# Performance work log

Hardware: AMD Instinct MI355X
Metric: run time of the kernel (lower is better)

The kernel has to match this reference:

```python
import jax, jax.numpy as jnp
import numpy as np
from jax import lax

B, A, SEQ, FIN = 512, 16, 50, 6
H, H2, T, G, S = 256, 128, 60, 64, 6
GR0, GR1 = -50.0, 50.0
CELL = (GR1 - GR0) / G
NTYPES, EMB = 10, 16
NENC, NL = 5, 2

def setup_inputs() -> dict:
    key = jax.random.key(0)
    ks = jax.random.split(key, 40)
    def rn(k, shape, scale=0.05):
        return (jax.random.normal(k, shape) * scale).astype(jnp.float32)
    history = jax.random.normal(ks[0], (B, A, SEQ, FIN), dtype=jnp.float32)
    types = jax.random.randint(ks[1], (B,), 0, NTYPES)
    history = history.at[:, 0, 0, 5].set(types.astype(jnp.float32))
    d = dict(history=history)
    d['emb'] = rn(ks[2], (NTYPES, EMB))
    d['fe_W1'] = rn(ks[3], (FIN + EMB, H)); d['fe_b1'] = jnp.zeros((H,), jnp.float32)
    d['fe_W2'] = rn(ks[4], (H, H));        d['fe_b2'] = jnp.zeros((H,), jnp.float32)
    d['enc_Wih'] = rn(ks[5], (NENC, NL, H, 3 * H))
    d['enc_Whh'] = rn(ks[6], (NENC, NL, H, 3 * H))
    d['enc_bih'] = rn(ks[7], (NENC, NL, 3 * H))
    d['enc_bhh'] = rn(ks[8], (NENC, NL, 3 * H))
    d['dec_Wih0'] = rn(ks[9], (2, 3 * H)); d['dec_Whh0'] = rn(ks[10], (H, 3 * H))
    d['dec_bih0'] = rn(ks[11], (3 * H));   d['dec_bhh0'] = rn(ks[12], (3 * H))
    d['dec_Wih1'] = rn(ks[13], (H, 3 * H)); d['dec_Whh1'] = rn(ks[14], (H, 3 * H))
    d['dec_bih1'] = rn(ks[15], (3 * H));    d['dec_bhh1'] = rn(ks[16], (3 * H))
    d['hg_W1'] = rn(ks[17], (H, H));   d['hg_b1'] = jnp.zeros((H,), jnp.float32)
    d['hg_W2'] = rn(ks[18], (H, H2));  d['hg_b2'] = jnp.zeros((H2,), jnp.float32)
    d['hg_W3'] = rn(ks[19], (H2, T * 2)); d['hg_b3'] = jnp.zeros((T * 2,), jnp.float32)
    d['ce_W1'] = rn(ks[20], (H, H2));  d['ce_b1'] = jnp.zeros((H2,), jnp.float32)
    d['ce_W2'] = rn(ks[21], (H2, T));  d['ce_b2'] = jnp.zeros((T,), jnp.float32)
    d['hp_W1'] = rn(ks[22], (H, H));   d['hp_b1'] = jnp.zeros((H,), jnp.float32)
    d['hp_W2'] = rn(ks[23], (H, G * G)); d['hp_b2'] = jnp.zeros((G * G,), jnp.float32)
    return d

def _gru_cell(xt, h, Wih, Whh, bih, bhh):
    # torch GRU gate order: r, z, n
    gi = xt @ Wih + bih
    gh = h @ Whh + bhh
    Hd = h.shape[-1]
    r = jax.nn.sigmoid(gi[:, :Hd] + gh[:, :Hd])
    z = jax.nn.sigmoid(gi[:, Hd:2 * Hd] + gh[:, Hd:2 * Hd])
    n = jnp.tanh(gi[:, 2 * Hd:] + r * gh[:, 2 * Hd:])
    return (1.0 - z) * n + z * h

def _forward(history, emb, fe_W1, fe_b1, fe_W2, fe_b2,
             enc_Wih, enc_Whh, enc_bih, enc_bhh,
             dec_Wih0, dec_Whh0, dec_bih0, dec_bhh0,
             dec_Wih1, dec_Whh1, dec_bih1, dec_bhh1,
             hg_W1, hg_b1, hg_W2, hg_b2, hg_W3, hg_b3,
             ce_W1, ce_b1, ce_W2, ce_b2, hp_W1, hp_b1, hp_W2, hp_b2):
    ego = history[:, 0]                                   # [B,SEQ,6]
    etype = jnp.clip(ego[:, 0, 5].astype(jnp.int32), 0, 9)
    # type -> encoder index (vehicle,pedestrian,cyclist,bus,default)
    eidx = jnp.array([0, 1, 4, 2, 3, 4, 4, 4, 4, 4], jnp.int32)[etype]
    te = emb[etype]                                       # [B,16]
    x_in = jnp.concatenate([ego, jnp.broadcast_to(te[:, None, :], (B, SEQ, EMB))], axis=-1)
    feat = jax.nn.relu(x_in @ fe_W1 + fe_b1) @ fe_W2 + fe_b2  # [B,SEQ,H]

    # 2-layer GRU with per-example (type-gathered) weights
    x_cur = feat.transpose(1, 0, 2)                       # [SEQ,B,H]
    h_finals = []
    for l in range(NL):
        Wih = enc_Wih[eidx, l]; Whh = enc_Whh[eidx, l]    # [B,H,3H]
        bih = enc_bih[eidx, l]; bhh = enc_bhh[eidx, l]    # [B,3H]
        def step(h, xt, Wih=Wih, Whh=Whh, bih=bih, bhh=bhh):
            gi = jnp.einsum('bd,bdg->bg', xt, Wih) + bih
            gh = jnp.einsum('bh,bhg->bg', h, Whh) + bhh
            r = jax.nn.sigmoid(gi[:, :H] + gh[:, :H])
            z = jax.nn.sigmoid(gi[:, H:2 * H] + gh[:, H:2 * H])
            n = jnp.tanh(gi[:, 2 * H:] + r * gh[:, 2 * H:])
            hn = (1.0 - z) * n + z * h
            return hn, hn
        h_last, ys = lax.scan(step, jnp.zeros((B, H), feat.dtype), x_cur)
        x_cur = ys
        h_finals.append(h_last)
    enc_h0, enc_h1 = h_finals

    # decoder GRU, single timestep: x = last ego position
    x0 = ego[:, -1, :2]
    h0 = _gru_cell(x0, enc_h0, dec_Wih0, dec_Whh0, dec_bih0, dec_bhh0)
    h1 = _gru_cell(h0, enc_h1, dec_Wih1, dec_Whh1, dec_bih1, dec_bhh1)
    last_hidden = h1                                      # [B,H]

    traj = (jax.nn.relu(jax.nn.relu(last_hidden @ hg_W1 + hg_b1) @ hg_W2 + hg_b2) @ hg_W3 + hg_b3)
    traj = traj.reshape(B, T, 2)
    conf = jax.nn.relu(last_hidden @ ce_W1 + ce_b1) @ ce_W2 + ce_b2   # [B,T]

    key = jax.random.key(42)
    k_noise, k_samp = jax.random.split(key)
    noise = jax.random.normal(k_noise, (T, B, H), last_hidden.dtype)
    scale = (0.1 * jnp.arange(T, dtype=last_hidden.dtype) / T)[:, None, None]
    th = last_hidden[None] + noise * scale                # [T,B,H]
    logits = jax.nn.relu(th @ hp_W1 + hp_b1) @ hp_W2 + hp_b2  # [T,B,G*G]

    # vectorized multinomial over (samples, timesteps, batch)
    idx = jax.random.categorical(k_samp, logits, shape=(S - 1, T, B))  # int [S-1,T,B]
    x_idx = (idx % G).astype(jnp.float32)
    y_idx = (idx // G).astype(jnp.float32)
    pts = jnp.stack([GR0 + x_idx * CELL + CELL / 2,
                     GR0 + y_idx * CELL + CELL / 2], axis=-1)  # [S-1,T,B,2]
    pts = pts.transpose(2, 0, 1, 3)                       # [B,S-1,T,2]

    predictions = jnp.concatenate([traj[:, None], pts], axis=1)  # [B,S,T,2]
    decay = jnp.float32(0.9) ** jnp.arange(S, dtype=jnp.float32)
    confidences = conf.mean(axis=1)[:, None] * decay[None, :]    # [B,S]
    return predictions, confidences

def reference(history, emb, fe_W1, fe_b1, fe_W2, fe_b2,
              enc_Wih, enc_Whh, enc_bih, enc_bhh,
              dec_Wih0, dec_Whh0, dec_bih0, dec_bhh0,
              dec_Wih1, dec_Whh1, dec_bih1, dec_bhh1,
              hg_W1, hg_b1, hg_W2, hg_b2, hg_W3, hg_b3,
              ce_W1, ce_b1, ce_W2, ce_b2, hp_W1, hp_b1, hp_W2, hp_b2):
    return _forward(history, emb, fe_W1, fe_b1, fe_W2, fe_b2,
                    enc_Wih, enc_Whh, enc_bih, enc_bhh,
                    dec_Wih0, dec_Whh0, dec_bih0, dec_bhh0,
                    dec_Wih1, dec_Whh1, dec_bih1, dec_bhh1,
                    hg_W1, hg_b1, hg_W2, hg_b2, hg_W3, hg_b3,
                    ce_W1, ce_b1, ce_W2, ce_b2, hp_W1, hp_b1, hp_W2, hp_b2)
```

## Files before the change

### kernel.cpp

```cpp
#include <hip/hip_runtime.h>
#include <stdint.h>
#include <math.h>

#define JAX_PARTITIONABLE 1

#define B_ 512
#define SEQ_ 50
#define H_ 256
#define H2_ 128
#define T_ 60
#define S_ 6
#define EMB_ 16
#define NL_ 2
#define TG_ 768
#define CAT_ 4096
#define GUMBEL_N 629145600u
#define NOISE_N 7864320u

__host__ __device__ inline void tf2x32(uint32_t k0, uint32_t k1, uint32_t x0, uint32_t x1,
                                       uint32_t& o0, uint32_t& o1) {
  uint32_t ks2 = k0 ^ k1 ^ 0x1BD11BDAu;
  x0 += k0; x1 += k1;
#define TFR(r) do { x0 += x1; x1 = (x1 << r) | (x1 >> (32 - r)); x1 ^= x0; } while (0)
  TFR(13); TFR(15); TFR(26); TFR(6);
  x0 += k1; x1 += ks2 + 1u;
  TFR(17); TFR(29); TFR(16); TFR(24);
  x0 += ks2; x1 += k0 + 2u;
  TFR(13); TFR(15); TFR(26); TFR(6);
  x0 += k0; x1 += k1 + 3u;
  TFR(17); TFR(29); TFR(16); TFR(24);
  x0 += k1; x1 += ks2 + 4u;
  TFR(13); TFR(15); TFR(26); TFR(6);
  x0 += ks2; x1 += k0 + 5u;
#undef TFR
  o0 = x0; o1 = x1;
}

__device__ inline uint32_t jax_bits(uint32_t k0, uint32_t k1, uint32_t i, uint32_t n) {
#if JAX_PARTITIONABLE
  (void)n;
  uint32_t a, b;
  tf2x32(k0, k1, 0u, i, a, b);
  return a ^ b;
#else
  uint32_t half = n >> 1;
  uint32_t lo = (i < half) ? i : (i - half);
  uint32_t a, b;
  tf2x32(k0, k1, lo, lo + half, a, b);
  return (i < half) ? a : b;
#endif
}

__device__ inline float bits_to_f01(uint32_t bits) {
  return __uint_as_float((bits >> 9) | 0x3f800000u) - 1.0f;
}

__device__ inline float erfinv_f(float x) {
  double xd = (double)x;
  float w = (float)(-log((1.0 - xd) * (1.0 + xd)));
  float p;
  if (w < 5.0f) {
    w = __fadd_rn(w, -2.5f);
    p = 2.81022636e-08f;
    p = __fadd_rn(3.43273939e-07f, __fmul_rn(p, w));
    p = __fadd_rn(-3.5233877e-06f, __fmul_rn(p, w));
    p = __fadd_rn(-4.39150654e-06f, __fmul_rn(p, w));
    p = __fadd_rn(0.00021858087f, __fmul_rn(p, w));
    p = __fadd_rn(-0.00125372503f, __fmul_rn(p, w));
    p = __fadd_rn(-0.00417768164f, __fmul_rn(p, w));
    p = __fadd_rn(0.246640727f, __fmul_rn(p, w));
    p = __fadd_rn(1.50140941f, __fmul_rn(p, w));
  } else {
    w = __fadd_rn(__fsqrt_rn(w), -3.0f);
    p = -0.000200214257f;
    p = __fadd_rn(0.000100950558f, __fmul_rn(p, w));
    p = __fadd_rn(0.00134934322f, __fmul_rn(p, w));
    p = __fadd_rn(-0.00367342844f, __fmul_rn(p, w));
    p = __fadd_rn(0.00573950773f, __fmul_rn(p, w));
    p = __fadd_rn(-0.0076224613f, __fmul_rn(p, w));
    p = __fadd_rn(0.00943887047f, __fmul_rn(p, w));
    p = __fadd_rn(1.00167406f, __fmul_rn(p, w));
    p = __fadd_rn(2.83297682f, __fmul_rn(p, w));
  }
  return __fmul_rn(p, x);
}

__device__ inline float gumbel_f32(uint32_t bits) {
  float f = bits_to_f01(bits);
  float u = fmaxf(f, 1.17549435e-38f);
  float l1 = logf(u);
  float g = -logf(-l1);
  return g;
}

__device__ inline uint32_t orderkey(float s) {
  uint32_t sb = __float_as_uint(s);
  return (sb & 0x80000000u) ? ~sb : (sb | 0x80000000u);
}

__global__ __launch_bounds__(512) void k_init(const float* __restrict__ hist,
                                              float* __restrict__ x0buf, int* __restrict__ ip) {
  int b = threadIdx.x;
  if (b < B_) {
    float tv = hist[b * 4800 + 5];
    int et = (int)tv;
    et = et < 0 ? 0 : (et > 9 ? 9 : et);
    const int mp[10] = {0, 1, 4, 2, 3, 4, 4, 4, 4, 4};
    ip[b] = et;
    ip[512 + b] = mp[et];
    x0buf[b * 2 + 0] = hist[b * 4800 + 49 * 6 + 0];
    x0buf[b * 2 + 1] = hist[b * 4800 + 49 * 6 + 1];
  }
  __syncthreads();
  if (b == 0) {
    int cnt[5] = {0, 0, 0, 0, 0};
    for (int i = 0; i < B_; i++) cnt[ip[512 + i]]++;
    int off[6];
    off[0] = 0;
    for (int e = 0; e < 5; e++) off[e + 1] = off[e] + cnt[e];
    int pos[5];
    for (int e = 0; e < 5; e++) pos[e] = off[e];
    for (int i = 0; i < B_; i++) { int e = ip[512 + i]; ip[1024 + pos[e]++] = i; }
    int* tbl = ip + 1536;
    int nrt = 0;
    for (int e = 0; e < 5; e++) {
      int n = cnt[e];
      for (int s = 0; s < n; s += 16) {
        tbl[1 + nrt] = e;
        tbl[37 + nrt] = off[e] + s;
        tbl[73 + nrt] = (n - s) < 16 ? (n - s) : 16;
        nrt++;
      }
    }
    tbl[0] = nrt;
  }
}

__global__ void k_zero(uint32_t* p, int n) {
  int i = blockIdx.x * blockDim.x + threadIdx.x;
  if (i < n) p[i] = 0u;
}

__global__ __launch_bounds__(256) void k_feat(const float* __restrict__ hist, const float* __restrict__ emb,
    const float* __restrict__ W1, const float* __restrict__ b1,
    const float* __restrict__ W2, const float* __restrict__ b2,
    const int* __restrict__ ip, float* __restrict__ featbuf) {
  __shared__ float xs[16][22];
  __shared__ float t1[16][H_];
  int row0 = blockIdx.x * 16;
  int tid = threadIdx.x;
  for (int idx = tid; idx < 16 * 22; idx += 256) {
    int r = idx / 22, c = idx % 22;
    int g = row0 + r;
    int b = g / SEQ_, s = g % SEQ_;
    xs[r][c] = (c < 6) ? hist[b * 4800 + s * 6 + c] : emb[ip[b] * EMB_ + (c - 6)];
  }
  __syncthreads();
  int j = tid;
  {
    double acc[16];
    for (int r = 0; r < 16; r++) acc[r] = 0.0;
    for (int k = 0; k < 22; k++) {
      double w = (double)W1[k * H_ + j];
      for (int r = 0; r < 16; r++) acc[r] += (double)xs[r][k] * w;
    }
    double bb = (double)b1[j];
    for (int r = 0; r < 16; r++) t1[r][j] = fmaxf((float)(acc[r] + bb), 0.0f);
  }
  __syncthreads();
  {
    double acc[16];
    for (int r = 0; r < 16; r++) acc[r] = 0.0;
    for (int k = 0; k < H_; k++) {
      double w = (double)W2[k * H_ + j];
      for (int r = 0; r < 16; r++) acc[r] += (double)t1[r][k] * w;
    }
    double bb = (double)b2[j];
    for (int r = 0; r < 16; r++) {
      float v = (float)(acc[r] + bb);
      int g = row0 + r;
      int b = g / SEQ_, s = g % SEQ_;
      featbuf[(size_t)s * (B_ * H_) + (size_t)b * H_ + j] = v;
    }
  }
}

__device__ __forceinline__ void gi_block(float (*xs)[H_], int* rowb,
    int rt, int cg, int tid,
    const float* __restrict__ x, float* __restrict__ gi_out,
    const float* __restrict__ Wih_base, const float* __restrict__ bih_base,
    int layer, const int* __restrict__ ip) {
  const int* tbl = ip + 1536;
  const int* order = ip + 1024;
  int nrt = tbl[0];
  if (rt >= nrt) return;
  int e = tbl[1 + rt];
  int start = tbl[37 + rt];
  int nr = tbl[73 + rt];
  for (int idx = tid; idx < 16 * H_; idx += 256) {
    int r = idx >> 8, k = idx & 255;
    int rr = (r < nr) ? r : 0;
    int b = order[start + rr];
    if (k == 0) rowb[r] = b;
    xs[r][k] = x[b * H_ + k];
  }
  __syncthreads();
  size_t woff = (size_t)(e * NL_ + layer);
  const float* Wih = Wih_base + woff * (size_t)H_ * TG_;
  const float* bih = bih_base + woff * TG_;
  int j = tid & 31, rs = tid >> 5;
  int c = cg * 32 + j;
  int cr = c, cz = H_ + c, cn = 2 * H_ + c;
  double ar0 = 0, ar1 = 0, az0 = 0, az1 = 0, an0 = 0, an1 = 0;
  for (int k = 0; k < H_; k++) {
    float wr = Wih[k * TG_ + cr], wz = Wih[k * TG_ + cz], wn = Wih[k * TG_ + cn];
    float x0 = xs[rs][k], x1 = xs[rs + 8][k];
    ar0 += (double)x0 * wr; ar1 += (double)x1 * wr;
    az0 += (double)x0 * wz; az1 += (double)x1 * wz;
    an0 += (double)x0 * wn; an1 += (double)x1 * wn;
  }
  double br = (double)bih[cr], bz = (double)bih[cz], bn = (double)bih[cn];
  for (int p = 0; p < 2; p++) {
    int r = rs + 8 * p;
    if (r >= nr) continue;
    int b = rowb[r];
    gi_out[b * TG_ + cr] = (float)((p ? ar1 : ar0) + br);
    gi_out[b * TG_ + cz] = (float)((p ? az1 : az0) + bz);
    gi_out[b * TG_ + cn] = (float)((p ? an1 : an0) + bn);
  }
}

__device__ __forceinline__ void step_block(float (*hs)[H_], int* rowb,
    int rt, int cg, int tid,
    const float* __restrict__ gi_in, const float* __restrict__ hin,
    float* __restrict__ hout, float* __restrict__ ys,
    const float* __restrict__ Whh_base, const float* __restrict__ bhh_base,
    int layer, const int* __restrict__ ip) {
  const int* tbl = ip + 1536;
  const int* order = ip + 1024;
  int nrt = tbl[0];
  if (rt >= nrt) return;
  int e = tbl[1 + rt];
  int start = tbl[37 + rt];
  int nr = tbl[73 + rt];
  for (int idx = tid; idx < 16 * H_; idx += 256) {
    int r = idx >> 8, k = idx & 255;
    int rr = (r < nr) ? r : 0;
    int b = order[start + rr];
    if (k == 0) rowb[r] = b;
    hs[r][k] = hin[b * H_ + k];
  }
  __syncthreads();
  size_t woff = (size_t)(e * NL_ + layer);
  const float* Whh = Whh_base + woff * (size_t)H_ * TG_;
  const float* bhh = bhh_base + woff * TG_;
  int j = tid & 31, rs = tid >> 5;
  int c = cg * 32 + j;
  int cr = c, cz = H_ + c, cn = 2 * H_ + c;
  double gr0 = 0, gr1 = 0, gz0 = 0, gz1 = 0, gn0 = 0, gn1 = 0;
  for (int k = 0; k < H_; k++) {
    float wr = Whh[k * TG_ + cr], wz = Whh[k * TG_ + cz], wn = Whh[k * TG_ + cn];
    float h0 = hs[rs][k], h1 = hs[rs + 8][k];
    gr0 += (double)h0 * wr; gr1 += (double)h1 * wr;
    gz0 += (double)h0 * wz; gz1 += (double)h1 * wz;
    gn0 += (double)h0 * wn; gn1 += (double)h1 * wn;
  }
  double bhr = (double)bhh[cr], bhz = (double)bhh[cz], bhn = (double)bhh[cn];
  for (int p = 0; p < 2; p++) {
    int r = rs + 8 * p;
    if (r >= nr) continue;
    int b = rowb[r];
    double gir = (double)gi_in[b * TG_ + cr];
    double giz = (double)gi_in[b * TG_ + cz];
    double gin = (double)gi_in[b * TG_ + cn];
    double ghr = (p ? gr1 : gr0) + bhr;
    double ghz = (p ? gz1 : gz0) + bhz;
    double ghn = (p ? gn1 : gn0) + bhn;
    double rr = 1.0 / (1.0 + exp(-(gir + ghr)));
    double zz = 1.0 / (1.0 + exp(-(giz + ghz)));
    double nn = tanh(gin + rr * ghn);
    double hv = (double)hs[r][c];
    float hnew = (float)((1.0 - zz) * nn + zz * hv);
    hout[b * H_ + c] = hnew;
    if (ys) ys[b * H_ + c] = hnew;
  }
}

__global__ __launch_bounds__(256) void k_pipe(int d,
    const float* __restrict__ feat, float* __restrict__ ys0,
    float* __restrict__ gi0, float* __restrict__ gi1,
    float* __restrict__ h0A, float* __restrict__ h0B,
    float* __restrict__ h1A, float* __restrict__ h1B,
    const float* __restrict__ Wih, const float* __restrict__ Whh,
    const float* __restrict__ bih, const float* __restrict__ bhh,
    const int* __restrict__ ip) {
  __shared__ float sb[16][H_];
  __shared__ int rowb[16];
  int g = blockIdx.x;
  int grp = g / 288, bx = g % 288;
  int rt = bx >> 3, cg = bx & 7;
  int tid = threadIdx.x;
  if (grp == 0) {
    int t = d; if (t >= SEQ_) return;
    gi_block(sb, rowb, rt, cg, tid, feat + (size_t)t * 131072,
             gi0 + (size_t)(t & 1) * 393216, Wih, bih, 0, ip);
  } else if (grp == 1) {
    int t = d - 1; if (t < 0 || t >= SEQ_) return;
    const float* hin = (t & 1) ? h0B : h0A;
    float* hout = (t & 1) ? h0A : h0B;
    step_block(sb, rowb, rt, cg, tid, gi0 + (size_t)(t & 1) * 393216,
               hin, hout, ys0 + (size_t)t * 131072, Whh, bhh, 0, ip);
  } else if (grp == 2) {
    int t = d - 2; if (t < 0 || t >= SEQ_) return;
    gi_block(sb, rowb, rt, cg, tid, ys0 + (size_t)t * 131072,
             gi1 + (size_t)(t & 1) * 393216, Wih, bih, 1, ip);
  } else {
    int t = d - 3; if (t < 0 || t >= SEQ_) return;
    const float* hin = (t & 1) ? h1B : h1A;
    float* hout = (t & 1) ? h1A : h1B;
    step_block(sb, rowb, rt, cg, tid, gi1 + (size_t)(t & 1) * 393216,
               hin, hout, nullptr, Whh, bhh, 1, ip);
  }
}

template <int D1>
__global__ __launch_bounds__(256) void k_gru(
    const float* __restrict__ x, const float* __restrict__ hin,
    float* __restrict__ hout,
    const float* __restrict__ Wih, const float* __restrict__ Whh,
    const float* __restrict__ bih, const float* __restrict__ bhh) {
  __shared__ float xs[16][(D1 == 2) ? 2 : H_];
  __shared__ float hs[16][H_];
  int bx = blockIdx.x, by = blockIdx.y;
  int start = bx * 16;
  int tid = threadIdx.x;
  for (int idx = tid; idx < 16 * H_; idx += 256) {
    int r = idx >> 8, k = idx & 255;
    int b = start + r;
    hs[r][k] = hin[b * H_ + k];
    if (D1 == H_) xs[r][k] = x[b * H_ + k];
    else if (k < D1) xs[r][k] = x[b * D1 + k];
  }
  __syncthreads();
  int j = tid & 31, rs = tid >> 5;
  int hc = by * 32 + j;
  int cr = hc, cz = H_ + hc, cn = 2 * H_ + hc;
  double ra0 = 0, ra1 = 0, za0 = 0, za1 = 0, ni0 = 0, ni1 = 0, nh0 = 0, nh1 = 0;
  for (int k = 0; k < H_; k++) {
    float wrh = Whh[k * TG_ + cr], wzh = Whh[k * TG_ + cz], wnh = Whh[k * TG_ + cn];
    float h0v = hs[rs][k], h1v = hs[rs + 8][k];
    ra0 += (double)h0v * wrh; ra1 += (double)h1v * wrh;
    za0 += (double)h0v * wzh; za1 += (double)h1v * wzh;
    nh0 += (double)h0v * wnh; nh1 += (double)h1v * wnh;
    if (D1 == H_) {
      float wri = Wih[k * TG_ + cr], wzi = Wih[k * TG_ + cz], wni = Wih[k * TG_ + cn];
      float x0v = xs[rs][k], x1v = xs[rs + 8][k];
      ra0 += (double)x0v * wri; ra1 += (double)x1v * wri;
      za0 += (double)x0v * wzi; za1 += (double)x1v * wzi;
      ni0 += (double)x0v * wni; ni1 += (double)x1v * wni;
    }
  }
  if (D1 != H_) {
    for (int k = 0; k < D1; k++) {
      float wri = Wih[k * TG_ + cr], wzi = Wih[k * TG_ + cz], wni = Wih[k * TG_ + cn];
      float x0v = xs[rs][k], x1v = xs[rs + 8][k];
      ra0 += (double)x0v * wri; ra1 += (double)x1v * wri;
      za0 += (double)x0v * wzi; za1 += (double)x1v * wzi;
      ni0 += (double)x0v * wni; ni1 += (double)x1v * wni;
    }
  }
  double br_i = (double)bih[cr], bz_i = (double)bih[cz], bn_i = (double)bih[cn];
  double br_h = (double)bhh[cr], bz_h = (double)bhh[cz], bn_h = (double)bhh[cn];
  for (int p = 0; p < 2; p++) {
    int r = rs + 8 * p;
    double ra = p ? ra1 : ra0, za = p ? za1 : za0, ni = p ? ni1 : ni0, nh = p ? nh1 : nh0;
    double rr = 1.0 / (1.0 + exp(-(ra + br_i + br_h)));
    double zz = 1.0 / (1.0 + exp(-(za + bz_i + bz_h)));
    double nn = tanh((ni + bn_i) + rr * (nh + bn_h));
    double hv = (double)hs[r][hc];
    float hnew = (float)((1.0 - zz) * nn + zz * hv);
    hout[(start + r) * H_ + hc] = hnew;
  }
}

__global__ __launch_bounds__(256) void k_heads(const float* __restrict__ lh,
    const float* __restrict__ hgW1, const float* __restrict__ hgb1,
    const float* __restrict__ hgW2, const float* __restrict__ hgb2,
    const float* __restrict__ hgW3, const float* __restrict__ hgb3,
    const float* __restrict__ ceW1, const float* __restrict__ ceb1,
    const float* __restrict__ ceW2, const float* __restrict__ ceb2,
    float* __restrict__ out) {
  __shared__ float hsm[16][H_];
  __shared__ float t1[16][H_];
  __shared__ float t2[16][H2_];
  __shared__ float c2s[16][T_];
  int row0 = blockIdx.x * 16;
  int tid = threadIdx.x;
  for (int idx = tid; idx < 16 * H_; idx += 256) {
    int r = idx >> 8, k = idx & 255;
    hsm[r][k] = lh[(size_t)(row0 + r) * H_ + k];
  }
  __syncthreads();
  {
    int j = tid;
    for (int r = 0; r < 16; r++) {
      double a = 0;
      for (int k = 0; k < H_; k++) a += (double)hsm[r][k] * (double)hgW1[k * H_ + j];
      t1[r][j] = fmaxf((float)(a + (double)hgb1[j]), 0.0f);
    }
  }
  __syncthreads();
  if (tid < H2_) {
    int j = tid;
    for (int r = 0; r < 16; r++) {
      double a = 0;
      for (int k = 0; k < H_; k++) a += (double)t1[r][k] * (double)hgW2[k * H2_ + j];
      t2[r][j] = fmaxf((float)(a + (double)hgb2[j]), 0.0f);
    }
  }
  __syncthreads();
  if (tid < 2 * T_) {
    int j = tid;
    for (int r = 0; r < 16; r++) {
      double a = 0;
      for (int k = 0; k < H2_; k++) a += (double)t2[r][k] * (double)hgW3[k * (2 * T_) + j];
      float v = (float)(a + (double)hgb3[j]);
      int b = row0 + r;
      int t = j >> 1, c = j & 1;
      out[(((size_t)b * S_ + 0) * T_ + t) * 2 + c] = v;
    }
  }
  __syncthreads();
  if (tid < H2_) {
    int j = tid;
    for (int r = 0; r < 16; r++) {
      double a = 0;
      for (int k = 0; k < H_; k++) a += (double)hsm[r][k] * (double)ceW1[k * H2_ + j];
      t2[r][j] = fmaxf((float)(a + (double)ceb1[j]), 0.0f);
    }
  }
  __syncthreads();
  if (tid < T_) {
    int j = tid;
    for (int r = 0; r < 16; r++) {
      double a = 0;
      for (int k = 0; k < H2_; k++) a += (double)t2[r][k] * (double)ceW2[k * T_ + j];
      c2s[r][j] = (float)(a + (double)ceb2[j]);
    }
  }
  __syncthreads();
  if (tid < 16) {
    int r = tid;
    int b = row0 + r;
    double s = 0;
    for (int j = 0; j < T_; j++) s += (double)c2s[r][j];
    float m = (float)(s / 60.0);
    for (int sd = 0; sd < S_; sd++) {
      float d = (float)pow((double)0.9f, (double)sd);
      out[368640 + b * S_ + sd] = __fmul_rn(m, d);
    }
  }
}

__global__ __launch_bounds__(256) void k_hp1(const float* __restrict__ lh,
    const float* __restrict__ W1, const float* __restrict__ b1,
    float* __restrict__ h1buf, uint32_t nk0, uint32_t nk1) {
  __shared__ float th[16][H_];
  int row0 = blockIdx.x * 16;
  int tid = threadIdx.x;
  const float SQRT2F = 1.4142135623730951f;
  const float LO = -0x1.fffffep-1f;
  for (int idx = tid; idx < 16 * H_; idx += 256) {
    int r = idx >> 8, k = idx & 255;
    int g = row0 + r;
    int t = g / B_, b = g % B_;
    uint32_t i = ((uint32_t)t * B_ + (uint32_t)b) * H_ + (uint32_t)k;
    uint32_t bits = jax_bits(nk0, nk1, i, NOISE_N);
    float f = bits_to_f01(bits);
    float u = fmaxf(LO, __fadd_rn(__fmul_rn(f, 2.0f), LO));
    float nz = __fmul_rn(SQRT2F, erfinv_f(u));
    float sc = __fdiv_rn(__fmul_rn(0.1f, (float)t), 60.0f);
    th[r][k] = __fadd_rn(lh[(size_t)b * H_ + k], __fmul_rn(nz, sc));
  }
  __syncthreads();
  int j = tid;
  double acc[16];
  for (int r = 0; r < 16; r++) acc[r] = 0.0;
  for (int k = 0; k < H_; k++) {
    double w = (double)W1[k * H_ + j];
    for (int r = 0; r < 16; r++) acc[r] += (double)th[r][k] * w;
  }
  double bb = (double)b1[j];
  for (int r = 0; r < 16; r++)
    h1buf[(size_t)(row0 + r) * H_ + j] = fmaxf((float)(acc[r] + bb), 0.0f);
}

__global__ __launch_bounds__(256) void k_hp2(const float* __restrict__ h1buf,
    const float* __restrict__ W2, const float* __restrict__ b2,
    unsigned long long* __restrict__ samples, uint32_t sk0, uint32_t sk1) {
  __shared__ float h1[16][H_];
  int row0 = blockIdx.x * 16;
  int cat0 = blockIdx.y * 128;
  int tid = threadIdx.x;
  for (int idx = tid; idx < 16 * H_ / 4; idx += 256) {
    int r = idx >> 6, k4 = (idx & 63) << 2;
    *(float4*)&h1[r][k4] = *(const float4*)&h1buf[(size_t)(row0 + r) * H_ + k4];
  }
  __syncthreads();
  int wave = tid >> 6;
  int lane = tid & 63;
  int catA = cat0 + 2 * lane;
  int rbase = 4 * wave;

  float acc[4][2];
  for (int q = 0; q < 4; q++) { acc[q][0] = 0.0f; acc[q][1] = 0.0f; }
  const float* w2p = W2 + catA;
  for (int k = 0; k < H_; k += 4) {
    float4 hv0 = *(const float4*)&h1[rbase + 0][k];
    float4 hv1 = *(const float4*)&h1[rbase + 1][k];
    float4 hv2 = *(const float4*)&h1[rbase + 2][k];
    float4 hv3 = *(const float4*)&h1[rbase + 3][k];
#pragma unroll
    for (int kk = 0; kk < 4; kk++) {
      float2 w = *(const float2*)&w2p[(size_t)(k + kk) * CAT_];
      float h0 = (&hv0.x)[kk], h1v = (&hv1.x)[kk], h2 = (&hv2.x)[kk], h3 = (&hv3.x)[kk];
      acc[0][0] = __fmaf_rn(h0, w.x, acc[0][0]); acc[0][1] = __fmaf_rn(h0, w.y, acc[0][1]);
      acc[1][0] = __fmaf_rn(h1v, w.x, acc[1][0]); acc[1][1] = __fmaf_rn(h1v, w.y, acc[1][1]);
      acc[2][0] = __fmaf_rn(h2, w.x, acc[2][0]); acc[2][1] = __fmaf_rn(h2, w.y, acc[2][1]);
      acc[3][0] = __fmaf_rn(h3, w.x, acc[3][0]); acc[3][1] = __fmaf_rn(h3, w.y, acc[3][1]);
    }
  }
  float lg[4][2];
  float b0 = b2[catA], b1v = b2[catA + 1];
  for (int q = 0; q < 4; q++) {
    lg[q][0] = __fadd_rn(acc[q][0], b0);
    lg[q][1] = __fadd_rn(acc[q][1], b1v);
  }

  int t = row0 / B_;
  int bbase = row0 % B_;
#pragma unroll
  for (int s = 0; s < S_ - 1; s++) {
#pragma unroll
    for (int q = 0; q < 4; q++) {
      int brow = bbase + rbase + q;
      uint32_t ibase = (((uint32_t)s * T_ + (uint32_t)t) * B_ + (uint32_t)brow) * CAT_ + (uint32_t)catA;
      float g0 = gumbel_f32(jax_bits(sk0, sk1, ibase, GUMBEL_N));
      float g1 = gumbel_f32(jax_bits(sk0, sk1, ibase + 1u, GUMBEL_N));
      float s0 = __fadd_rn(g0, lg[q][0]);
      float s1 = __fadd_rn(g1, lg[q][1]);
      uint32_t k0 = orderkey(s0), k1 = orderkey(s1);
      uint32_t bestk; int bestc;
      if (k1 > k0) { bestk = k1; bestc = catA + 1; }
      else         { bestk = k0; bestc = catA; }
      uint32_t m = bestk;
      for (int off = 1; off < 64; off <<= 1) {
        uint32_t o = __shfl_xor(m, off, 64);
        m = m > o ? m : o;
      }
      unsigned long long mask = __ballot(bestk == m);
      int src = __ffsll(mask) - 1;
      int wcat = __shfl(bestc, src, 64);
      if (lane == 0) {
        unsigned long long p =
            (((unsigned long long)m) << 32) | (unsigned long long)(~(uint32_t)wcat);
        atomicMax(&samples[((size_t)s * T_ + t) * B_ + brow], p);
      }
    }
  }
}

__global__ void k_emit(const unsigned long long* __restrict__ samples, float* __restrict__ out) {
  int gid = blockIdx.x * blockDim.x + threadIdx.x;
  if (gid >= (S_ - 1) * T_ * B_) return;
  int b = gid % B_;
  int t = (gid / B_) % T_;
  int s = gid / (B_ * T_);
  unsigned long long v = samples[gid];
  uint32_t cat = ~(uint32_t)(v & 0xFFFFFFFFu);
  float xi = (float)(cat & 63u);
  float yi = (float)(cat >> 6);
  float px = -50.0f + xi * 1.5625f + 0.78125f;
  float py = -50.0f + yi * 1.5625f + 0.78125f;
  size_t o = (((size_t)b * S_ + (size_t)(s + 1)) * T_ + t) * 2;
  out[o] = px;
  out[o + 1] = py;
}

extern "C" void kernel_launch(void* const* d_in, const int* in_sizes, int n_in,
                              void* d_out, int out_size, void* d_ws, size_t ws_size,
                              hipStream_t stream) {
  (void)in_sizes; (void)n_in; (void)out_size; (void)ws_size;
  const float* hist   = (const float*)d_in[0];
  const float* emb    = (const float*)d_in[1];
  const float* feW1   = (const float*)d_in[2];
  const float* feb1   = (const float*)d_in[3];
  const float* feW2   = (const float*)d_in[4];
  const float* feb2   = (const float*)d_in[5];
  const float* encWih = (const float*)d_in[6];
  const float* encWhh = (const float*)d_in[7];
  const float* encbih = (const float*)d_in[8];
  const float* encbhh = (const float*)d_in[9];
  const float* dWih0  = (const float*)d_in[10];
  const float* dWhh0  = (const float*)d_in[11];
  const float* dbih0  = (const float*)d_in[12];
  const float* dbhh0  = (const float*)d_in[13];
  const float* dWih1  = (const float*)d_in[14];
  const float* dWhh1  = (const float*)d_in[15];
  const float* dbih1  = (const float*)d_in[16];
  const float* dbhh1  = (const float*)d_in[17];
  const float* hgW1   = (const float*)d_in[18];
  const float* hgb1   = (const float*)d_in[19];
  const float* hgW2   = (const float*)d_in[20];
  const float* hgb2   = (const float*)d_in[21];
  const float* hgW3   = (const float*)d_in[22];
  const float* hgb3   = (const float*)d_in[23];
  const float* ceW1   = (const float*)d_in[24];
  const float* ceb1   = (const float*)d_in[25];
  const float* ceW2   = (const float*)d_in[26];
  const float* ceb2   = (const float*)d_in[27];
  const float* hpW1   = (const float*)d_in[28];
  const float* hpb1   = (const float*)d_in[29];
  const float* hpW2   = (const float*)d_in[30];
  const float* hpb2   = (const float*)d_in[31];
  float* out = (float*)d_out;
  float* ws = (float*)d_ws;

  float* feat  = ws;
  float* ys0   = ws + 6553600;
  float* gi0   = ws + 13107200;
  float* gi1   = ws + 13893632;
  float* h0A   = ws + 14680064;
  float* h0B   = h0A + 131072;
  float* h1A   = h0B + 131072;
  float* h1B   = h1A + 131072;
  float* dech0 = h1B + 131072;
  float* lh    = dech0 + 131072;
  float* x0buf = lh + 131072;
  int*   ip    = (int*)(x0buf + 1024);
  unsigned long long* samples =
      (unsigned long long*)(((uintptr_t)(ip + 2048) + 255) & ~(uintptr_t)255);
  float* h1hp  = ws;

  uint32_t kn0, kn1, ks0, ks1;
#if JAX_PARTITIONABLE
  tf2x32(0u, 42u, 0u, 0u, kn0, kn1);
  tf2x32(0u, 42u, 0u, 1u, ks0, ks1);
#else
  { uint32_t a0, a1, b0, b1;
    tf2x32(0u, 42u, 0u, 2u, a0, a1);
    tf2x32(0u, 42u, 1u, 3u, b0, b1);
    kn0 = a0; kn1 = b0; ks0 = a1; ks1 = b1; }
#endif

  k_init<<<dim3(1), dim3(512), 0, stream>>>(hist, x0buf, ip);
  k_zero<<<dim3((524288 + 255) / 256), dim3(256), 0, stream>>>((uint32_t*)h0A, 524288);
  k_zero<<<dim3((307200 + 255) / 256), dim3(256), 0, stream>>>((uint32_t*)samples, 307200);
  k_feat<<<dim3(1600), dim3(256), 0, stream>>>(hist, emb, feW1, feb1, feW2, feb2, ip, feat);

  for (int d = 0; d < SEQ_ + 3; d++) {
    k_pipe<<<dim3(1152), dim3(256), 0, stream>>>(d,
        feat, ys0, gi0, gi1, h0A, h0B, h1A, h1B,
        encWih, encWhh, encbih, encbhh, ip);
  }

  k_gru<2><<<dim3(32, 8), dim3(256), 0, stream>>>(
      x0buf, h0A, dech0, dWih0, dWhh0, dbih0, dbhh0);
  k_gru<H_><<<dim3(32, 8), dim3(256), 0, stream>>>(
      dech0, h1A, lh, dWih1, dWhh1, dbih1, dbhh1);

  k_heads<<<dim3(32), dim3(256), 0, stream>>>(lh, hgW1, hgb1, hgW2, hgb2, hgW3, hgb3,
                                              ceW1, ceb1, ceW2, ceb2, out);
  k_hp1<<<dim3(1920), dim3(256), 0, stream>>>(lh, hpW1, hpb1, h1hp, kn0, kn1);
  k_hp2<<<dim3(1920, 32), dim3(256), 0, stream>>>(h1hp, hpW2, hpb2, samples, ks0, ks1);
  k_emit<<<dim3(600), dim3(256), 0, stream>>>(samples, out);
}
```

Baseline: 6.115 ms.

## Widen hp2 tiles to four categories per lane with packed FMA and alignbit rotates

```diff
diff --git a/kernel.cpp b/kernel.cpp
--- a/kernel.cpp
+++ b/kernel.cpp
@@ -17,11 +17,26 @@
 #define GUMBEL_N 629145600u
 #define NOISE_N 7864320u
 
+typedef float f32x2 __attribute__((ext_vector_type(2)));
+
+#define PKFMA_LO(acc, w, h) \
+  asm("v_pk_fma_f32 %0, %1, %2, %0 op_sel:[0,0,0] op_sel_hi:[1,0,1]" : "+v"(acc) : "v"(w), "v"(h))
+#define PKFMA_HI(acc, w, h) \
+  asm("v_pk_fma_f32 %0, %1, %2, %0 op_sel:[0,1,0] op_sel_hi:[1,1,1]" : "+v"(acc) : "v"(w), "v"(h))
+
+__host__ __device__ inline uint32_t rotl32(uint32_t x, int r) {
+#if defined(__HIP_DEVICE_COMPILE__)
+  return __builtin_amdgcn_alignbit(x, x, 32 - r);
+#else
+  return (x << r) | (x >> (32 - r));
+#endif
+}
+
 __host__ __device__ inline void tf2x32(uint32_t k0, uint32_t k1, uint32_t x0, uint32_t x1,
                                        uint32_t& o0, uint32_t& o1) {
   uint32_t ks2 = k0 ^ k1 ^ 0x1BD11BDAu;
   x0 += k0; x1 += k1;
-#define TFR(r) do { x0 += x1; x1 = (x1 << r) | (x1 >> (32 - r)); x1 ^= x0; } while (0)
+#define TFR(r) do { x0 += x1; x1 = rotl32(x1, r); x1 ^= x0; } while (0)
   TFR(13); TFR(15); TFR(26); TFR(6);
   x0 += k1; x1 += ks2 + 1u;
   TFR(17); TFR(29); TFR(16); TFR(24);
@@ -89,8 +104,7 @@
   float f = bits_to_f01(bits);
   float u = fmaxf(f, 1.17549435e-38f);
   float l1 = logf(u);
-  float g = -logf(-l1);
-  return g;
+  return -logf(-l1);
 }
 
 __device__ inline uint32_t orderkey(float s) {
@@ -500,7 +514,7 @@
     unsigned long long* __restrict__ samples, uint32_t sk0, uint32_t sk1) {
   __shared__ float h1[16][H_];
   int row0 = blockIdx.x * 16;
-  int cat0 = blockIdx.y * 128;
+  int cat0 = blockIdx.y * 256;
   int tid = threadIdx.x;
   for (int idx = tid; idx < 16 * H_ / 4; idx += 256) {
     int r = idx >> 6, k4 = (idx & 63) << 2;
@@ -509,32 +523,44 @@
   __syncthreads();
   int wave = tid >> 6;
   int lane = tid & 63;
-  int catA = cat0 + 2 * lane;
+  int catA = cat0 + 4 * lane;
   int rbase = 4 * wave;
 
-  float acc[4][2];
-  for (int q = 0; q < 4; q++) { acc[q][0] = 0.0f; acc[q][1] = 0.0f; }
+  f32x2 acc[4][2];
+#pragma unroll
+  for (int r = 0; r < 4; r++) { acc[r][0] = (f32x2)0.0f; acc[r][1] = (f32x2)0.0f; }
   const float* w2p = W2 + catA;
   for (int k = 0; k < H_; k += 4) {
-    float4 hv0 = *(const float4*)&h1[rbase + 0][k];
-    float4 hv1 = *(const float4*)&h1[rbase + 1][k];
-    float4 hv2 = *(const float4*)&h1[rbase + 2][k];
-    float4 hv3 = *(const float4*)&h1[rbase + 3][k];
+    float4 hv[4];
+    hv[0] = *(const float4*)&h1[rbase + 0][k];
+    hv[1] = *(const float4*)&h1[rbase + 1][k];
+    hv[2] = *(const float4*)&h1[rbase + 2][k];
+    hv[3] = *(const float4*)&h1[rbase + 3][k];
+    float4 wv[4];
+#pragma unroll
+    for (int kk = 0; kk < 4; kk++) wv[kk] = *(const float4*)&w2p[(size_t)(k + kk) * CAT_];
 #pragma unroll
     for (int kk = 0; kk < 4; kk++) {
-      float2 w = *(const float2*)&w2p[(size_t)(k + kk) * CAT_];
-      float h0 = (&hv0.x)[kk], h1v = (&hv1.x)[kk], h2 = (&hv2.x)[kk], h3 = (&hv3.x)[kk];
-      acc[0][0] = __fmaf_rn(h0, w.x, acc[0][0]); acc[0][1] = __fmaf_rn(h0, w.y, acc[0][1]);
-      acc[1][0] = __fmaf_rn(h1v, w.x, acc[1][0]); acc[1][1] = __fmaf_rn(h1v, w.y, acc[1][1]);
-      acc[2][0] = __fmaf_rn(h2, w.x, acc[2][0]); acc[2][1] = __fmaf_rn(h2, w.y, acc[2][1]);
-      acc[3][0] = __fmaf_rn(h3, w.x, acc[3][0]); acc[3][1] = __fmaf_rn(h3, w.y, acc[3][1]);
-    }
-  }
-  float lg[4][2];
-  float b0 = b2[catA], b1v = b2[catA + 1];
-  for (int q = 0; q < 4; q++) {
-    lg[q][0] = __fadd_rn(acc[q][0], b0);
-    lg[q][1] = __fadd_rn(acc[q][1], b1v);
+      f32x2 wlo; wlo.x = wv[kk].x; wlo.y = wv[kk].y;
+      f32x2 whi; whi.x = wv[kk].z; whi.y = wv[kk].w;
+#pragma unroll
+      for (int r = 0; r < 4; r++) {
+        f32x2 hp;
+        if (kk & 2) { hp.x = (&hv[r].x)[2]; hp.y = (&hv[r].x)[3]; }
+        else        { hp.x = (&hv[r].x)[0]; hp.y = (&hv[r].x)[1]; }
+        if (kk & 1) { PKFMA_HI(acc[r][0], wlo, hp); PKFMA_HI(acc[r][1], whi, hp); }
+        else        { PKFMA_LO(acc[r][0], wlo, hp); PKFMA_LO(acc[r][1], whi, hp); }
+      }
+    }
+  }
+  float lg[4][4];
+  float4 b4 = *(const float4*)&b2[catA];
+#pragma unroll
+  for (int r = 0; r < 4; r++) {
+    lg[r][0] = __fadd_rn(acc[r][0].x, b4.x);
+    lg[r][1] = __fadd_rn(acc[r][0].y, b4.y);
+    lg[r][2] = __fadd_rn(acc[r][1].x, b4.z);
+    lg[r][3] = __fadd_rn(acc[r][1].y, b4.w);
   }
 
   int t = row0 / B_;
@@ -545,25 +571,23 @@
     for (int q = 0; q < 4; q++) {
       int brow = bbase + rbase + q;
       uint32_t ibase = (((uint32_t)s * T_ + (uint32_t)t) * B_ + (uint32_t)brow) * CAT_ + (uint32_t)catA;
-      float g0 = gumbel_f32(jax_bits(sk0, sk1, ibase, GUMBEL_N));
-      float g1 = gumbel_f32(jax_bits(sk0, sk1, ibase + 1u, GUMBEL_N));
-      float s0 = __fadd_rn(g0, lg[q][0]);
-      float s1 = __fadd_rn(g1, lg[q][1]);
-      uint32_t k0 = orderkey(s0), k1 = orderkey(s1);
-      uint32_t bestk; int bestc;
-      if (k1 > k0) { bestk = k1; bestc = catA + 1; }
-      else         { bestk = k0; bestc = catA; }
-      uint32_t m = bestk;
-      for (int off = 1; off < 64; off <<= 1) {
-        uint32_t o = __shfl_xor(m, off, 64);
-        m = m > o ? m : o;
-      }
-      unsigned long long mask = __ballot(bestk == m);
+      float sc0 = __fadd_rn(gumbel_f32(jax_bits(sk0, sk1, ibase + 0u, GUMBEL_N)), lg[q][0]);
+      float sc1 = __fadd_rn(gumbel_f32(jax_bits(sk0, sk1, ibase + 1u, GUMBEL_N)), lg[q][1]);
+      float sc2 = __fadd_rn(gumbel_f32(jax_bits(sk0, sk1, ibase + 2u, GUMBEL_N)), lg[q][2]);
+      float sc3 = __fadd_rn(gumbel_f32(jax_bits(sk0, sk1, ibase + 3u, GUMBEL_N)), lg[q][3]);
+      float bs = sc0; int bc = catA;
+      if (sc1 > bs) { bs = sc1; bc = catA + 1; }
+      if (sc2 > bs) { bs = sc2; bc = catA + 2; }
+      if (sc3 > bs) { bs = sc3; bc = catA + 3; }
+      float mv = bs;
+      for (int off = 1; off < 64; off <<= 1)
+        mv = fmaxf(mv, __shfl_xor(mv, off, 64));
+      unsigned long long mask = __ballot(bs == mv);
       int src = __ffsll(mask) - 1;
-      int wcat = __shfl(bestc, src, 64);
+      int wcat = __shfl(bc, src, 64);
       if (lane == 0) {
         unsigned long long p =
-            (((unsigned long long)m) << 32) | (unsigned long long)(~(uint32_t)wcat);
+            (((unsigned long long)orderkey(mv)) << 32) | (unsigned long long)(~(uint32_t)wcat);
         atomicMax(&samples[((size_t)s * T_ + t) * B_ + brow], p);
       }
     }
@@ -672,6 +696,6 @@
   k_heads<<<dim3(32), dim3(256), 0, stream>>>(lh, hgW1, hgb1, hgW2, hgb2, hgW3, hgb3,
                                               ceW1, ceb1, ceW2, ceb2, out);
   k_hp1<<<dim3(1920), dim3(256), 0, stream>>>(lh, hpW1, hpb1, h1hp, kn0, kn1);
-  k_hp2<<<dim3(1920, 32), dim3(256), 0, stream>>>(h1hp, hpW2, hpb2, samples, ks0, ks1);
+  k_hp2<<<dim3(1920, 16), dim3(256), 0, stream>>>(h1hp, hpW2, hpb2, samples, ks0, ks1);
   k_emit<<<dim3(600), dim3(256), 0, stream>>>(samples, out);
 }
```

Result: faster. 5.837 ms (-4.5%).
